# Optimization experiments

Measured on AMD Instinct MI355X. Metric: run time of the kernel, lower is better.

The kernel has to match this reference:

```python
import jax, jax.numpy as jnp
import numpy as np

B, T, D = 2, 2048, 1024
H = 16
HD = D // H
SCALE = 1.0 / np.sqrt(HD).astype(np.float32)


def setup_inputs() -> dict:
    key = jax.random.key(0)
    ks = jax.random.split(key, 5)
    std = 1.0 / np.sqrt(D).astype(np.float32)
    x = jax.random.normal(ks[0], (B, T, D), dtype=jnp.float32)
    Wqkvt = jax.random.normal(ks[1], (D, 4 * D), dtype=jnp.float32) * std
    bqkvt = jax.random.normal(ks[2], (4 * D,), dtype=jnp.float32) * 0.02
    Wout = jax.random.normal(ks[3], (D, D), dtype=jnp.float32) * std
    bout = jax.random.normal(ks[4], (D,), dtype=jnp.float32) * 0.02
    return {"x": x, "Wqkvt": Wqkvt, "bqkvt": bqkvt, "Wout": Wout, "bout": bout}


def reference(x, Wqkvt, bqkvt, Wout, bout):
    b, t, d = x.shape
    # fused qkvt projection -> [B,T,4,H,HD]
    qkvt = (x @ Wqkvt + bqkvt).reshape(b, t, 4, H, HD)
    # -> [B,H,T,HD] each
    q, k, v, tt = [jnp.transpose(qkvt[:, :, i], (0, 2, 1, 3)) for i in range(4)]

    # standard dot-product scores [B,H,T,T]
    scores_dot = jnp.einsum('bhqd,bhkd->bhqk', q, k)
    # triplet term: (q*t) against cumsum over keys of (k*v)/sqrt(hd)
    kv = k * v * SCALE
    kv_cum = jnp.cumsum(kv, axis=2)  # causal prefix over key positions
    scores_trip = jnp.einsum('bhqd,bhkd->bhqk', q * tt, kv_cum)

    scores = (scores_dot + scores_trip) * SCALE
    causal = jnp.triu(jnp.ones((t, t), dtype=bool), k=1)
    scores = jnp.where(causal[None, None], -jnp.inf, scores)

    attn = jax.nn.softmax(scores, axis=-1)
    out = jnp.einsum('bhqk,bhkd->bhqd', attn, v)  # [B,H,T,HD]
    out = jnp.transpose(out, (0, 2, 1, 3)).reshape(b, t, d)
    return out @ Wout + bout
```

## Files before the change

kernel.cpp:

```cpp
#include <hip/hip_runtime.h>

#define T_SEQ 2048
#define D_MODEL 1024
#define NH 16
#define HD 64
#define BH_TOT 32
#define M_ROWS 4096
#define NT 32
#define SCALE 0.125f
#define BHT (BH_TOT * T_SEQ)
#define LOG2E 1.44269504f
#define TAU 2.885f

typedef _Float16 h8 __attribute__((ext_vector_type(8)));
typedef _Float16 h4 __attribute__((ext_vector_type(4)));
typedef float f32x4 __attribute__((ext_vector_type(4)));

__device__ __forceinline__ f32x4 mfma_h(h8 a, h8 b, f32x4 c) {
    return __builtin_amdgcn_mfma_f32_16x16x32_f16(a, b, c, 0, 0, 0);
}

__device__ __forceinline__ void gload16(const _Float16* g, _Float16* l) {
    __builtin_amdgcn_global_load_lds(
        (const __attribute__((address_space(1))) unsigned int*)g,
        (__attribute__((address_space(3))) unsigned int*)l, 16, 0, 0);
}

__global__ void k_convert(const float* __restrict__ in, _Float16* __restrict__ out, int n) {
    int i = (blockIdx.x * blockDim.x + threadIdx.x) * 4;
    if (i < n) {
        float4 v = *(const float4*)(in + i);
        h4 o;
        o[0] = (_Float16)v.x; o[1] = (_Float16)v.y;
        o[2] = (_Float16)v.z; o[3] = (_Float16)v.w;
        *(h4*)(out + i) = o;
    }
}

__global__ void k_transpose(const float* __restrict__ in, _Float16* __restrict__ out, int K, int N) {
    __shared__ float tile[32][33];
    int nb = blockIdx.x * 32, kb = blockIdx.y * 32;
    int tx = threadIdx.x & 31, ty = threadIdx.x >> 5;
    #pragma unroll
    for (int i = 0; i < 32; i += 8)
        tile[ty + i][tx] = in[(size_t)(kb + ty + i) * N + (nb + tx)];
    __syncthreads();
    #pragma unroll
    for (int i = 0; i < 32; i += 8)
        out[(size_t)(nb + ty + i) * K + (kb + tx)] = (_Float16)tile[tx][ty + i];
}

template<int MODE>
__launch_bounds__(256, 2)
__global__ void k_gemm(const _Float16* __restrict__ A, const _Float16* __restrict__ Bt,
                       int M, int N, int K, const float* __restrict__ bias,
                       _Float16* __restrict__ qo, _Float16* __restrict__ keo,
                       _Float16* __restrict__ vo, _Float16* __restrict__ vto,
                       _Float16* __restrict__ to, float* __restrict__ cOut)
{
    __shared__ __align__(16) _Float16 lA[128 * 64];
    __shared__ __align__(16) _Float16 lB[128 * 64];
    const int tid = threadIdx.x;
    const int wid = tid >> 6, lane = tid & 63, lrow = lane & 15, lg = lane >> 4;
    const int wm = wid >> 1, wn = wid & 1;
    const int m0 = blockIdx.x * 128, n0 = blockIdx.y * 128;

    f32x4 acc[4][4];
    #pragma unroll
    for (int i = 0; i < 4; i++)
        #pragma unroll
        for (int j = 0; j < 4; j++) acc[i][j] = (f32x4){0.f, 0.f, 0.f, 0.f};

    const int rin = lane >> 3, gcol = lane & 7;
    const int scol = (gcol ^ rin) * 8;
    const _Float16* gA = A + (size_t)(m0 + 32 * wid + rin) * K + scol;
    const _Float16* gB = Bt + (size_t)(n0 + 32 * wid + rin) * K + scol;
    _Float16* lAw = &lA[32 * wid * 64];
    _Float16* lBw = &lB[32 * wid * 64];

    const int r7 = lrow & 7;
    const int nk = K >> 6;
    for (int kt = 0; kt < nk; ++kt) {
        const size_t ko = (size_t)kt * 64;
        #pragma unroll
        for (int i = 0; i < 4; i++) {
            gload16(gA + (size_t)(8 * i) * K + ko, lAw + 8 * i * 64);
            gload16(gB + (size_t)(8 * i) * K + ko, lBw + 8 * i * 64);
        }
        __syncthreads();

        h8 af[4][2], bfr[4][2];
        #pragma unroll
        for (int mi = 0; mi < 4; mi++) {
            const int row = wm * 64 + mi * 16 + lrow;
            af[mi][0] = *(const h8*)&lA[row * 64 + ((lg ^ r7) * 8)];
            af[mi][1] = *(const h8*)&lA[row * 64 + (((4 + lg) ^ r7) * 8)];
        }
        #pragma unroll
        for (int ni = 0; ni < 4; ni++) {
            const int row = wn * 64 + ni * 16 + lrow;
            bfr[ni][0] = *(const h8*)&lB[row * 64 + ((lg ^ r7) * 8)];
            bfr[ni][1] = *(const h8*)&lB[row * 64 + (((4 + lg) ^ r7) * 8)];
        }
        #pragma unroll
        for (int mi = 0; mi < 4; mi++)
            #pragma unroll
            for (int ni = 0; ni < 4; ni++) {
                acc[mi][ni] = mfma_h(af[mi][0], bfr[ni][0], acc[mi][ni]);
                acc[mi][ni] = mfma_h(af[mi][1], bfr[ni][1], acc[mi][ni]);
            }
        __syncthreads();
    }

    if (MODE == 0) {
        const int ssel = n0 >> 10;
        #pragma unroll
        for (int mi = 0; mi < 4; mi++) {
            #pragma unroll
            for (int ni = 0; ni < 4; ni++) {
                const int nn = n0 + wn * 64 + ni * 16 + lrow;
                const float bv = bias[nn];
                const int h = (nn >> 6) & 15, hd = nn & 63;
                const int mmb = m0 + wm * 64 + mi * 16 + 4 * lg;
                const int b = mmb >> 11, t0 = mmb & (T_SEQ - 1);
                const size_t rowb = (size_t)(b * NH + h) * T_SEQ;
                h4 hv;
                #pragma unroll
                for (int r = 0; r < 4; r++) hv[r] = (_Float16)(acc[mi][ni][r] + bv);
                if (ssel == 0) {
                    #pragma unroll
                    for (int r = 0; r < 4; r++) qo[(rowb + t0 + r) * HD + hd] = hv[r];
                } else if (ssel == 1) {
                    #pragma unroll
                    for (int r = 0; r < 4; r++) keo[(rowb + t0 + r) * 128 + hd] = hv[r];
                } else if (ssel == 2) {
                    #pragma unroll
                    for (int r = 0; r < 4; r++) vo[(rowb + t0 + r) * HD + hd] = hv[r];
                    *(h4*)&vto[((size_t)(b * NH + h) * HD + hd) * T_SEQ + t0] = hv;
                } else {
                    #pragma unroll
                    for (int r = 0; r < 4; r++) to[(rowb + t0 + r) * HD + hd] = hv[r];
                }
            }
        }
    } else {
        #pragma unroll
        for (int mi = 0; mi < 4; mi++) {
            #pragma unroll
            for (int ni = 0; ni < 4; ni++) {
                const int nn = n0 + wn * 64 + ni * 16 + lrow;
                const float bv = bias[nn];
                #pragma unroll
                for (int r = 0; r < 4; r++) {
                    const int mm = m0 + wm * 64 + mi * 16 + 4 * lg + r;
                    cOut[(size_t)mm * N + nn] = acc[mi][ni][r] + bv;
                }
            }
        }
    }
}

__global__ void k_kvcum(_Float16* __restrict__ Ke, const _Float16* __restrict__ Vb)
{
    const int bh = blockIdx.x;
    const int w = threadIdx.x >> 6, lane = threadIdx.x & 63;
    const size_t bk = (size_t)bh * T_SEQ * 128 + lane;
    const size_t bv = (size_t)bh * T_SEQ * HD + lane;
    const int CH = T_SEQ / 16;
    const int t0 = w * CH;
    float s = 0.f;
    for (int i = 0; i < CH; i++)
        s += (float)Ke[bk + (size_t)(t0 + i) * 128] * (float)Vb[bv + (size_t)(t0 + i) * HD];
    __shared__ float tot[16][64];
    tot[w][lane] = s;
    __syncthreads();
    float acc = 0.f;
    for (int ww = 0; ww < w; ww++) acc += tot[ww][lane];
    for (int i = 0; i < CH; i++) {
        size_t ok = bk + (size_t)(t0 + i) * 128;
        acc += (float)Ke[ok] * (float)Vb[bv + (size_t)(t0 + i) * HD];
        Ke[ok + 64] = (_Float16)(acc * SCALE);
    }
}

__launch_bounds__(256, 4)
__global__ void k_attn(const _Float16* __restrict__ Qb, const _Float16* __restrict__ Ke,
                       const _Float16* __restrict__ Vt, const _Float16* __restrict__ Tb,
                       _Float16* __restrict__ Op0, _Float16* __restrict__ Op1,
                       _Float16* __restrict__ Op2, _Float16* __restrict__ Op3,
                       float* __restrict__ ML, int nsplit)
{
    const int bh = blockIdx.x;
    const int pair = blockIdx.y;
    const int ksel = blockIdx.z;
    const int tid = threadIdx.x;
    const int wid = tid >> 6, lane = tid & 63, lrow = lane & 15, lg = lane >> 4;
    const _Float16* qp = Qb + (size_t)bh * T_SEQ * HD;
    const _Float16* kep = Ke + (size_t)bh * T_SEQ * 128;
    const _Float16* tp = Tb + (size_t)bh * T_SEQ * HD;
    const _Float16* vp = Vt + (size_t)bh * T_SEQ * HD;
    _Float16* op = (ksel == 0) ? Op0 : (ksel == 1) ? Op1 : (ksel == 2) ? Op2 : Op3;
    float* ml = ML + (size_t)ksel * BHT * 2;

    __shared__ __align__(16) _Float16 ldsK[64 * 128];
    __shared__ __align__(16) _Float16 ldsV[64 * 64];
    __shared__ __align__(16) _Float16 lP[4][16 * 64];

    const int kpos = tid & 15, kprow = tid >> 4;
    const int vpos = tid & 7,  vprow = tid >> 3;
    const int r7 = lrow & 7;
    int kswz[4];
    #pragma unroll
    for (int c = 0; c < 4; c++) kswz[c] = ((c * 4 + lg) ^ r7) * 8;

    const h8 ones = {(_Float16)1.f, (_Float16)1.f, (_Float16)1.f, (_Float16)1.f,
                     (_Float16)1.f, (_Float16)1.f, (_Float16)1.f, (_Float16)1.f};
    const float C = SCALE * LOG2E;

    for (int half = 0; half < 2; ++half) {
        const int qi = half ? (NT - 1 - pair) : pair;
        const int q0 = qi * 64;
        const int nj = qi + 1;
        const int jbeg = (nj * ksel) / nsplit;
        const int jend = (nj * (ksel + 1)) / nsplit;

        const int qrow = q0 + wid * 16 + lrow;
        h8 qf[4];
        #pragma unroll
        for (int ks = 0; ks < 2; ++ks) {
            h8 qv = *(const h8*)&qp[(size_t)qrow * HD + ks * 32 + lg * 8];
            h8 tv = *(const h8*)&tp[(size_t)qrow * HD + ks * 32 + lg * 8];
            h8 a2, b2;
            #pragma unroll
            for (int i = 0; i < 8; i++) {
                float qq = (float)qv[i] * C;
                a2[i] = (_Float16)qq;
                b2[i] = (_Float16)(qq * (float)tv[i]);
            }
            qf[ks] = a2; qf[2 + ks] = b2;
        }

        float m_r[4];
        f32x4 o[4], o4;
        #pragma unroll
        for (int r = 0; r < 4; r++) m_r[r] = -__builtin_inff();
        #pragma unroll
        for (int ct = 0; ct < 4; ct++) o[ct] = (f32x4){0.f, 0.f, 0.f, 0.f};
        o4 = (f32x4){0.f, 0.f, 0.f, 0.f};

        h8 stK[4], stV[2];
        auto issue = [&](int j) {
            #pragma unroll
            for (int rr = 0; rr < 4; rr++)
                stK[rr] = *(const h8*)&kep[(size_t)(j * 64 + rr * 16 + kprow) * 128 + kpos * 8];
            #pragma unroll
            for (int rr = 0; rr < 2; rr++)
                stV[rr] = *(const h8*)&vp[(size_t)(rr * 32 + vprow) * T_SEQ + j * 64 + vpos * 8];
        };
        if (jbeg < jend) issue(jbeg);

        for (int j = jbeg; j < jend; ++j) {
            __syncthreads();
            #pragma unroll
            for (int rr = 0; rr < 4; rr++) {
                const int row = rr * 16 + kprow;
                *(h8*)&ldsK[row * 128 + ((kpos ^ (row & 7)) * 8)] = stK[rr];
            }
            #pragma unroll
            for (int rr = 0; rr < 2; rr++) {
                const int d = rr * 32 + vprow;
                *(h8*)&ldsV[d * 64 + ((vpos ^ (d & 7)) * 8)] = stV[rr];
            }
            __syncthreads();
            if (j + 1 < jend) issue(j + 1);

            f32x4 s[4];
            #pragma unroll
            for (int ct = 0; ct < 4; ct++) {
                const _Float16* kb = &ldsK[(ct * 16 + lrow) * 128];
                f32x4 sv = (f32x4){0.f, 0.f, 0.f, 0.f};
                sv = mfma_h(qf[0], *(const h8*)&kb[kswz[0]], sv);
                sv = mfma_h(qf[1], *(const h8*)&kb[kswz[1]], sv);
                sv = mfma_h(qf[2], *(const h8*)&kb[kswz[2]], sv);
                sv = mfma_h(qf[3], *(const h8*)&kb[kswz[3]], sv);
                s[ct] = sv;
            }
            if (j == qi) {
                #pragma unroll
                for (int ct = 0; ct < 4; ct++)
                    #pragma unroll
                    for (int r = 0; r < 4; r++) {
                        int key = j * 64 + ct * 16 + lrow;
                        int qr  = q0 + wid * 16 + 4 * lg + r;
                        if (key > qr) s[ct][r] = -__builtin_inff();
                    }
            }
            float mx[4];
            #pragma unroll
            for (int r = 0; r < 4; r++)
                mx[r] = fmaxf(fmaxf(s[0][r], s[1][r]), fmaxf(s[2][r], s[3][r]));
            bool need = (mx[0] > m_r[0] + TAU) | (mx[1] > m_r[1] + TAU) |
                        (mx[2] > m_r[2] + TAU) | (mx[3] > m_r[3] + TAU);
            if (__any(need)) {
                #pragma unroll
                for (int d = 1; d < 16; d <<= 1)
                    #pragma unroll
                    for (int r = 0; r < 4; r++) mx[r] = fmaxf(mx[r], __shfl_xor(mx[r], d, 64));
                #pragma unroll
                for (int r = 0; r < 4; r++) {
                    float mn = fmaxf(m_r[r], mx[r]);
                    float scl = __builtin_amdgcn_exp2f(m_r[r] - mn);
                    o[0][r] *= scl; o[1][r] *= scl; o[2][r] *= scl; o[3][r] *= scl;
                    o4[r] *= scl;
                    m_r[r] = mn;
                }
            }
            #pragma unroll
            for (int ct = 0; ct < 4; ct++) {
                const int col = ct * 16 + lrow;
                #pragma unroll
                for (int r = 0; r < 4; r++) {
                    float p = __builtin_amdgcn_exp2f(s[ct][r] - m_r[r]);
                    const int row = 4 * lg + r;
                    const int boff = row * 128 + ((col * 2) ^ ((row & 7) << 4));
                    lP[wid][boff >> 1] = (_Float16)p;
                }
            }
            h8 pa[2];
            #pragma unroll
            for (int ks = 0; ks < 2; ks++) {
                const int boff = lrow * 128 + ((ks * 64 + lg * 16) ^ ((lrow & 7) << 4));
                pa[ks] = *(const h8*)((const char*)lP[wid] + boff);
            }
            o4 = mfma_h(pa[0], ones, o4);
            o4 = mfma_h(pa[1], ones, o4);
            #pragma unroll
            for (int ct = 0; ct < 4; ct++) {
                const _Float16* vb = &ldsV[(ct * 16 + lrow) * 64];
                o[ct] = mfma_h(pa[0], *(const h8*)&vb[kswz[0]], o[ct]);
                o[ct] = mfma_h(pa[1], *(const h8*)&vb[kswz[1]], o[ct]);
            }
        }
        #pragma unroll
        for (int ct = 0; ct < 4; ct++)
            #pragma unroll
            for (int r = 0; r < 4; r++) {
                const int trow = q0 + wid * 16 + 4 * lg + r;
                const int d = ct * 16 + lrow;
                op[((size_t)bh * T_SEQ + trow) * HD + d] = (_Float16)o[ct][r];
            }
        if (lrow == 0) {
            #pragma unroll
            for (int r = 0; r < 4; r++) {
                const int trow = q0 + wid * 16 + 4 * lg + r;
                const size_t mi = ((size_t)bh * T_SEQ + trow) * 2;
                ml[mi] = m_r[r];
                ml[mi + 1] = o4[r];
            }
        }
    }
}

__global__ void k_combine(const _Float16* __restrict__ Op0, const _Float16* __restrict__ Op1,
                          const _Float16* __restrict__ Op2, const _Float16* __restrict__ Op3,
                          const float* __restrict__ ML, _Float16* __restrict__ AO, int nsplit)
{
    const int idx = blockIdx.x * 256 + threadIdx.x;
    const int row = idx >> 3;
    const int d0 = (idx & 7) * 8;
    const int bh = row >> 11, t = row & (T_SEQ - 1);
    const int b = bh >> 4, h = bh & 15;
    const _Float16* ops[4] = {Op0, Op1, Op2, Op3};
    float m = -__builtin_inff();
    for (int c = 0; c < nsplit; c++) m = fmaxf(m, ML[(size_t)c * BHT * 2 + 2 * row]);
    float w[4], denom = 0.f;
    for (int c = 0; c < nsplit; c++) {
        w[c] = __builtin_amdgcn_exp2f(ML[(size_t)c * BHT * 2 + 2 * row] - m);
        denom += w[c] * ML[(size_t)c * BHT * 2 + 2 * row + 1];
    }
    const float inv = 1.0f / denom;
    float accv[8];
    #pragma unroll
    for (int i = 0; i < 8; i++) accv[i] = 0.f;
    for (int c = 0; c < nsplit; c++) {
        h8 a = *(const h8*)&ops[c][(size_t)row * HD + d0];
        #pragma unroll
        for (int i = 0; i < 8; i++) accv[i] += w[c] * (float)a[i];
    }
    h8 r;
    #pragma unroll
    for (int i = 0; i < 8; i++) r[i] = (_Float16)(accv[i] * inv);
    *(h8*)&AO[((size_t)(b * T_SEQ + t)) * D_MODEL + h * HD + d0] = r;
}

extern "C" void kernel_launch(void* const* d_in, const int* in_sizes, int n_in,
                              void* d_out, int out_size, void* d_ws, size_t ws_size,
                              hipStream_t stream)
{
    const float* x     = (const float*)d_in[0];
    const float* Wqkvt = (const float*)d_in[1];
    const float* bqkvt = (const float*)d_in[2];
    const float* Wout  = (const float*)d_in[3];
    const float* bout  = (const float*)d_in[4];
    float* out = (float*)d_out;

    char* ws = (char*)d_ws;
    size_t off = 0;
    auto alloc = [&](size_t bytes) {
        char* p = ws + off;
        off += (bytes + 255) & ~(size_t)255;
        return p;
    };
    const size_t SZ = (size_t)M_ROWS * D_MODEL * 2;
    _Float16* xb  = (_Float16*)alloc(SZ);
    _Float16* wt  = (_Float16*)alloc(SZ);
    _Float16* wo  = (_Float16*)alloc((size_t)D_MODEL * D_MODEL * 2);
    _Float16* Qh  = (_Float16*)alloc(SZ);
    _Float16* Ke  = (_Float16*)alloc(SZ * 2);
    _Float16* Vh  = (_Float16*)alloc(SZ);
    _Float16* Vth = (_Float16*)alloc(SZ);
    _Float16* Th  = (_Float16*)alloc(SZ);
    _Float16* AO  = (_Float16*)alloc(SZ);
    const size_t need4 = off + 2 * SZ;
    _Float16* Op2 = (_Float16*)alloc(SZ);
    _Float16* Op3 = (_Float16*)alloc(SZ);

    const int nsplit = (ws_size >= need4) ? 4 : 2;

    _Float16* Op0 = xb;
    _Float16* Op1 = Vh;
    float*    ML  = (float*)wt;

    k_convert<<<4096, 256, 0, stream>>>(x, xb, M_ROWS * D_MODEL);
    k_transpose<<<dim3(128, 32), 256, 0, stream>>>(Wqkvt, wt, D_MODEL, 4 * D_MODEL);
    k_transpose<<<dim3(32, 32), 256, 0, stream>>>(Wout, wo, D_MODEL, D_MODEL);
    k_gemm<0><<<dim3(32, 32), 256, 0, stream>>>(xb, wt, M_ROWS, 4 * D_MODEL, D_MODEL,
                                                bqkvt, Qh, Ke, Vh, Vth, Th, nullptr);
    k_kvcum<<<BH_TOT, 1024, 0, stream>>>(Ke, Vh);
    k_attn<<<dim3(BH_TOT, NT / 2, nsplit), 256, 0, stream>>>(Qh, Ke, Vth, Th,
                                                             Op0, Op1, Op2, Op3, ML, nsplit);
    k_combine<<<BHT * HD / 8 / 256, 256, 0, stream>>>(Op0, Op1, Op2, Op3, ML, AO, nsplit);
    k_gemm<1><<<dim3(32, 8), 256, 0, stream>>>(AO, wo, M_ROWS, D_MODEL, D_MODEL,
                                               bout, nullptr, nullptr, nullptr, nullptr,
                                               nullptr, out);
}
```

Baseline: 191.4 us.

## Double-buffer LDS tiles with async global-to-LDS loads in GEMM and attention

The GEMM mainloop gets ping-pong LDS buffers, so the next K tile's global_load_lds is issued before the current tile is computed. In the attention kernel, the register-staged K/V copies are replaced by direct global-to-LDS loads into double buffers, with the XOR swizzle moved to the global address side and one barrier per iteration instead of two. The aim is to overlap memory latency with MFMA work and drop the VGPR staging. The cost is doubled LDS use, which lowers occupancy: k_attn's launch bounds drop from 4 to 2 blocks per CU. There is also a risk of missing waits before the next tile's LDS data is consumed.

```diff
diff --git a/kernel.cpp b/kernel.cpp
--- a/kernel.cpp
+++ b/kernel.cpp
@@ -58,8 +58,8 @@
                        _Float16* __restrict__ vo, _Float16* __restrict__ vto,
                        _Float16* __restrict__ to, float* __restrict__ cOut)
 {
-    __shared__ __align__(16) _Float16 lA[128 * 64];
-    __shared__ __align__(16) _Float16 lB[128 * 64];
+    __shared__ __align__(16) _Float16 lA[2][128 * 64];
+    __shared__ __align__(16) _Float16 lB[2][128 * 64];
     const int tid = threadIdx.x;
     const int wid = tid >> 6, lane = tid & 63, lrow = lane & 15, lg = lane >> 4;
     const int wm = wid >> 1, wn = wid & 1;
@@ -75,32 +75,39 @@
     const int scol = (gcol ^ rin) * 8;
     const _Float16* gA = A + (size_t)(m0 + 32 * wid + rin) * K + scol;
     const _Float16* gB = Bt + (size_t)(n0 + 32 * wid + rin) * K + scol;
-    _Float16* lAw = &lA[32 * wid * 64];
-    _Float16* lBw = &lB[32 * wid * 64];
 
     const int r7 = lrow & 7;
     const int nk = K >> 6;
+
+    #pragma unroll
+    for (int i = 0; i < 4; i++) {
+        gload16(gA + (size_t)(8 * i) * K, &lA[0][32 * wid * 64 + 8 * i * 64]);
+        gload16(gB + (size_t)(8 * i) * K, &lB[0][32 * wid * 64 + 8 * i * 64]);
+    }
+    __syncthreads();
+
     for (int kt = 0; kt < nk; ++kt) {
-        const size_t ko = (size_t)kt * 64;
-        #pragma unroll
-        for (int i = 0; i < 4; i++) {
-            gload16(gA + (size_t)(8 * i) * K + ko, lAw + 8 * i * 64);
-            gload16(gB + (size_t)(8 * i) * K + ko, lBw + 8 * i * 64);
-        }
-        __syncthreads();
-
+        const int cur = kt & 1;
+        if (kt + 1 < nk) {
+            const size_t ko = (size_t)(kt + 1) * 64;
+            #pragma unroll
+            for (int i = 0; i < 4; i++) {
+                gload16(gA + (size_t)(8 * i) * K + ko, &lA[cur ^ 1][32 * wid * 64 + 8 * i * 64]);
+                gload16(gB + (size_t)(8 * i) * K + ko, &lB[cur ^ 1][32 * wid * 64 + 8 * i * 64]);
+            }
+        }
         h8 af[4][2], bfr[4][2];
         #pragma unroll
         for (int mi = 0; mi < 4; mi++) {
             const int row = wm * 64 + mi * 16 + lrow;
-            af[mi][0] = *(const h8*)&lA[row * 64 + ((lg ^ r7) * 8)];
-            af[mi][1] = *(const h8*)&lA[row * 64 + (((4 + lg) ^ r7) * 8)];
+            af[mi][0] = *(const h8*)&lA[cur][row * 64 + ((lg ^ r7) * 8)];
+            af[mi][1] = *(const h8*)&lA[cur][row * 64 + (((4 + lg) ^ r7) * 8)];
         }
         #pragma unroll
         for (int ni = 0; ni < 4; ni++) {
             const int row = wn * 64 + ni * 16 + lrow;
-            bfr[ni][0] = *(const h8*)&lB[row * 64 + ((lg ^ r7) * 8)];
-            bfr[ni][1] = *(const h8*)&lB[row * 64 + (((4 + lg) ^ r7) * 8)];
+            bfr[ni][0] = *(const h8*)&lB[cur][row * 64 + ((lg ^ r7) * 8)];
+            bfr[ni][1] = *(const h8*)&lB[cur][row * 64 + (((4 + lg) ^ r7) * 8)];
         }
         #pragma unroll
         for (int mi = 0; mi < 4; mi++)
@@ -183,7 +190,7 @@
     }
 }
 
-__launch_bounds__(256, 4)
+__launch_bounds__(256, 2)
 __global__ void k_attn(const _Float16* __restrict__ Qb, const _Float16* __restrict__ Ke,
                        const _Float16* __restrict__ Vt, const _Float16* __restrict__ Tb,
                        _Float16* __restrict__ Op0, _Float16* __restrict__ Op1,
@@ -202,16 +209,31 @@
     _Float16* op = (ksel == 0) ? Op0 : (ksel == 1) ? Op1 : (ksel == 2) ? Op2 : Op3;
     float* ml = ML + (size_t)ksel * BHT * 2;
 
-    __shared__ __align__(16) _Float16 ldsK[64 * 128];
-    __shared__ __align__(16) _Float16 ldsV[64 * 64];
+    __shared__ __align__(16) _Float16 ldsK[2][64 * 128];
+    __shared__ __align__(16) _Float16 ldsV[2][64 * 64];
     __shared__ __align__(16) _Float16 lP[4][16 * 64];
 
-    const int kpos = tid & 15, kprow = tid >> 4;
-    const int vpos = tid & 7,  vprow = tid >> 3;
     const int r7 = lrow & 7;
     int kswz[4];
     #pragma unroll
     for (int c = 0; c < 4; c++) kswz[c] = ((c * 4 + lg) ^ r7) * 8;
+
+    const int krow4 = lane >> 4, kg = lane & 15;
+    const int vrow8 = lane >> 3, vg = lane & 7;
+    auto stage = [&](int j, int buf) {
+        #pragma unroll
+        for (int rr = 0; rr < 4; rr++) {
+            const int row = 16 * wid + rr * 4 + krow4;
+            gload16(&kep[(size_t)(j * 64 + row) * 128 + ((kg ^ (row & 7)) * 8)],
+                    &ldsK[buf][(16 * wid + rr * 4) * 128]);
+        }
+        #pragma unroll
+        for (int rr = 0; rr < 2; rr++) {
+            const int d = 16 * wid + rr * 8 + vrow8;
+            gload16(&vp[(size_t)d * T_SEQ + j * 64 + ((vg ^ (d & 7)) * 8)],
+                    &ldsV[buf][(16 * wid + rr * 8) * 64]);
+        }
+    };
 
     const h8 ones = {(_Float16)1.f, (_Float16)1.f, (_Float16)1.f, (_Float16)1.f,
                      (_Float16)1.f, (_Float16)1.f, (_Float16)1.f, (_Float16)1.f};
@@ -248,36 +270,17 @@
         for (int ct = 0; ct < 4; ct++) o[ct] = (f32x4){0.f, 0.f, 0.f, 0.f};
         o4 = (f32x4){0.f, 0.f, 0.f, 0.f};
 
-        h8 stK[4], stV[2];
-        auto issue = [&](int j) {
-            #pragma unroll
-            for (int rr = 0; rr < 4; rr++)
-                stK[rr] = *(const h8*)&kep[(size_t)(j * 64 + rr * 16 + kprow) * 128 + kpos * 8];
-            #pragma unroll
-            for (int rr = 0; rr < 2; rr++)
-                stV[rr] = *(const h8*)&vp[(size_t)(rr * 32 + vprow) * T_SEQ + j * 64 + vpos * 8];
-        };
-        if (jbeg < jend) issue(jbeg);
+        if (jbeg < jend) stage(jbeg, 0);
+        __syncthreads();
 
         for (int j = jbeg; j < jend; ++j) {
-            __syncthreads();
-            #pragma unroll
-            for (int rr = 0; rr < 4; rr++) {
-                const int row = rr * 16 + kprow;
-                *(h8*)&ldsK[row * 128 + ((kpos ^ (row & 7)) * 8)] = stK[rr];
-            }
-            #pragma unroll
-            for (int rr = 0; rr < 2; rr++) {
-                const int d = rr * 32 + vprow;
-                *(h8*)&ldsV[d * 64 + ((vpos ^ (d & 7)) * 8)] = stV[rr];
-            }
-            __syncthreads();
-            if (j + 1 < jend) issue(j + 1);
+            const int cur = (j - jbeg) & 1;
+            if (j + 1 < jend) stage(j + 1, cur ^ 1);
 
             f32x4 s[4];
             #pragma unroll
             for (int ct = 0; ct < 4; ct++) {
-                const _Float16* kb = &ldsK[(ct * 16 + lrow) * 128];
+                const _Float16* kb = &ldsK[cur][(ct * 16 + lrow) * 128];
                 f32x4 sv = (f32x4){0.f, 0.f, 0.f, 0.f};
                 sv = mfma_h(qf[0], *(const h8*)&kb[kswz[0]], sv);
                 sv = mfma_h(qf[1], *(const h8*)&kb[kswz[1]], sv);
@@ -336,10 +339,11 @@
             o4 = mfma_h(pa[1], ones, o4);
             #pragma unroll
             for (int ct = 0; ct < 4; ct++) {
-                const _Float16* vb = &ldsV[(ct * 16 + lrow) * 64];
+                const _Float16* vb = &ldsV[cur][(ct * 16 + lrow) * 64];
                 o[ct] = mfma_h(pa[0], *(const h8*)&vb[kswz[0]], o[ct]);
                 o[ct] = mfma_h(pa[1], *(const h8*)&vb[kswz[1]], o[ct]);
             }
+            __syncthreads();
         }
         #pragma unroll
         for (int ct = 0; ct < 4; ct++)
```

Result: no change. 190.8 us (-0.3%).
